# Optimization experiments

Hardware: AMD Instinct MI355X
Metric: run time of the kernel (lower is better)

The kernel has to match this reference:

```python
import jax, jax.numpy as jnp
import numpy as np

B, L1, L2, H = 32, 512, 512, 1024
NEG_INF = jnp.float32(-1e30)


def setup_inputs() -> dict:
    key = jax.random.key(0)
    k1, k2, k3, k4 = jax.random.split(key, 4)
    x1_bar = jax.random.normal(k1, (B, L1, H), dtype=jnp.float32)
    x2_bar = jax.random.normal(k2, (B, L2, H), dtype=jnp.float32)
    # lengths in [1, L] to avoid fully-masked (NaN) rows
    seq_lengths1 = jax.random.randint(k3, (B,), 1, L1 + 1, dtype=jnp.int32)
    seq_lengths2 = jax.random.randint(k4, (B,), 1, L2 + 1, dtype=jnp.int32)
    return {"x1_bar": x1_bar, "seq_lengths1": seq_lengths1,
            "x2_bar": x2_bar, "seq_lengths2": seq_lengths2}


def _enhance(x_bar, x_tilde):
    return jnp.concatenate([x_bar, x_tilde, x_bar - x_tilde, x_bar * x_tilde], axis=-1)


def reference(x1_bar, seq_lengths1, x2_bar, seq_lengths2):
    # e[b, i, j] = x1_bar[b, i] . x2_bar[b, j]
    e = jnp.einsum('bih,bjh->bij', x1_bar, x2_bar)  # [B, L1, L2]
    # mask_k[b, l] True where position l is padding (l >= length)
    mask1 = jnp.arange(x1_bar.shape[1])[None, :] >= seq_lengths1[:, None]  # [B, L1]
    mask2 = jnp.arange(x2_bar.shape[1])[None, :] >= seq_lengths2[:, None]  # [B, L2]
    # attend x1 -> x2: softmax over j with padded j masked
    a12 = jax.nn.softmax(jnp.where(mask2[:, None, :], NEG_INF, e), axis=2)  # [B, L1, L2]
    x1_tilde = jnp.einsum('bij,bjh->bih', a12, x2_bar)
    # attend x2 -> x1: softmax over i (on e^T) with padded i masked
    a21 = jax.nn.softmax(jnp.where(mask1[:, None, :], NEG_INF, e.transpose(0, 2, 1)), axis=2)  # [B, L2, L1]
    x2_tilde = jnp.einsum('bji,bih->bjh', a21, x1_bar)
    return _enhance(x1_bar, x1_tilde), _enhance(x2_bar, x2_tilde)
```

## Files before the change

### kernel.cpp

```cpp
#include <hip/hip_runtime.h>
#include <math.h>


namespace {

constexpr int BATCH = 32;
constexpr int L = 512;
constexpr int H = 1024;
constexpr int OUTH = 4 * H;

constexpr int BM = 128;
constexpr int BN = 128;
constexpr int KT = 32;
constexpr int LDSP = BM + 4;

__device__ __forceinline__ float wave_max(float v) {
#pragma unroll
  for (int off = 32; off > 0; off >>= 1) v = fmaxf(v, __shfl_xor(v, off));
  return v;
}
__device__ __forceinline__ float wave_sum(float v) {
#pragma unroll
  for (int off = 32; off > 0; off >>= 1) v += __shfl_xor(v, off);
  return v;
}

__global__ __launch_bounds__(256, 2)
void gemm_nt_kernel(const float* __restrict__ A, const float* __restrict__ Bm,
                    float* __restrict__ C) {
  __shared__ __align__(16) float As[KT][LDSP];
  __shared__ __align__(16) float Bs[KT][LDSP];
  const int b = blockIdx.z;
  const int m0 = blockIdx.x * BM;
  const int n0 = blockIdx.y * BN;
  const int tid = threadIdx.x;
  const float* Ab = A + (size_t)b * L * H + (size_t)m0 * H;
  const float* Bb = Bm + (size_t)b * L * H + (size_t)n0 * H;

  const int srow = tid >> 1;
  const int soff = (tid & 1) << 4;

  const int tm = tid & 15;
  const int tn = tid >> 4;

  float c[8][8];
#pragma unroll
  for (int i = 0; i < 8; ++i)
#pragma unroll
    for (int j = 0; j < 8; ++j) c[i][j] = 0.f;

  for (int k0 = 0; k0 < H; k0 += KT) {
    float4 av[4], bv[4];
    const float4* ap = (const float4*)(Ab + (size_t)srow * H + k0 + soff);
    const float4* bp = (const float4*)(Bb + (size_t)srow * H + k0 + soff);
#pragma unroll
    for (int q = 0; q < 4; ++q) av[q] = ap[q];
#pragma unroll
    for (int q = 0; q < 4; ++q) bv[q] = bp[q];
    __syncthreads();
#pragma unroll
    for (int q = 0; q < 4; ++q) {
      As[soff + q * 4 + 0][srow] = av[q].x;
      As[soff + q * 4 + 1][srow] = av[q].y;
      As[soff + q * 4 + 2][srow] = av[q].z;
      As[soff + q * 4 + 3][srow] = av[q].w;
      Bs[soff + q * 4 + 0][srow] = bv[q].x;
      Bs[soff + q * 4 + 1][srow] = bv[q].y;
      Bs[soff + q * 4 + 2][srow] = bv[q].z;
      Bs[soff + q * 4 + 3][srow] = bv[q].w;
    }
    __syncthreads();
#pragma unroll
    for (int k = 0; k < KT; ++k) {
      float a[8], bb[8];
      *(float4*)&a[0] = *(const float4*)&As[k][tm * 4];
      *(float4*)&a[4] = *(const float4*)&As[k][64 + tm * 4];
      *(float4*)&bb[0] = *(const float4*)&Bs[k][tn * 4];
      *(float4*)&bb[4] = *(const float4*)&Bs[k][64 + tn * 4];
#pragma unroll
      for (int i = 0; i < 8; ++i)
#pragma unroll
        for (int j = 0; j < 8; ++j) c[i][j] = fmaf(a[i], bb[j], c[i][j]);
    }
  }

  float* Cb = C + (size_t)b * L * L;
#pragma unroll
  for (int i = 0; i < 8; ++i) {
    const int m = m0 + ((i < 4) ? (tm * 4 + i) : (64 + tm * 4 + (i - 4)));
    float4 v0 = make_float4(c[i][0], c[i][1], c[i][2], c[i][3]);
    float4 v1 = make_float4(c[i][4], c[i][5], c[i][6], c[i][7]);
    *(float4*)(Cb + (size_t)m * L + n0 + tn * 4) = v0;
    *(float4*)(Cb + (size_t)m * L + n0 + 64 + tn * 4) = v1;
  }
}

__global__ __launch_bounds__(256)
void col_stats_partial_kernel(const float* __restrict__ e, const int* __restrict__ len1,
                              float* __restrict__ pm, float* __restrict__ ps) {
  const int b = blockIdx.y;
  const int j = blockIdx.x * 256 + threadIdx.x;
  const int ch = blockIdx.z;
  const int n1 = len1[b];
  const int i0 = ch * (L / 4);
  const int i1 = min(n1, i0 + L / 4);
  const float* eb = e + (size_t)b * L * L + j;
  float m = -INFINITY, s = 0.f;
  for (int i = i0; i < i1; ++i) {
    float v = eb[(size_t)i * L];
    float nm = fmaxf(m, v);
    s = s * __expf(m - nm) + __expf(v - nm);
    m = nm;
  }
  const int idx = (ch * BATCH + b) * L + j;
  pm[idx] = m;
  ps[idx] = s;
}

__global__ __launch_bounds__(256)
void col_stats_combine_kernel(const float* __restrict__ pm, const float* __restrict__ ps,
                              float* __restrict__ cmax, float* __restrict__ crcp) {
  const int idx = blockIdx.x * 256 + threadIdx.x;
  float m = -INFINITY;
#pragma unroll
  for (int c = 0; c < 4; ++c) m = fmaxf(m, pm[c * (BATCH * L) + idx]);
  float s = 0.f;
#pragma unroll
  for (int c = 0; c < 4; ++c) {
    float mc = pm[c * (BATCH * L) + idx];
    float sc = ps[c * (BATCH * L) + idx];
    s += (mc == -INFINITY) ? 0.f : sc * __expf(mc - m);
  }
  cmax[idx] = m;
  crcp[idx] = 1.f / s;
}

__global__ __launch_bounds__(256)
void transpose_softmax_kernel(const float* __restrict__ e, const float* __restrict__ cmax,
                              const float* __restrict__ crcp, const int* __restrict__ len1,
                              float* __restrict__ p21) {
  __shared__ float t[64][65];
  const int b = blockIdx.z;
  const int i0 = blockIdx.x << 6;
  const int j0 = blockIdx.y << 6;
  const int cc = threadIdx.x & 63;
  const int rr = threadIdx.x >> 6;
  const float* eb = e + (size_t)b * L * L;
#pragma unroll
  for (int ch = 0; ch < 16; ++ch) {
    const int r = (ch << 2) + rr;
    t[r][cc] = eb[(size_t)(i0 + r) * L + j0 + cc];
  }
  __syncthreads();
  const int n1 = len1[b];
  float* pb = p21 + (size_t)b * L * L;
#pragma unroll
  for (int ch = 0; ch < 16; ++ch) {
    const int r = (ch << 2) + rr;
    const int j = j0 + r;
    const float mj = cmax[b * L + j];
    const float rj = crcp[b * L + j];
    const int i = i0 + cc;
    const float val = (i < n1) ? __expf(t[cc][r] - mj) * rj : 0.f;
    pb[(size_t)j * L + i] = val;
  }
}

__global__ __launch_bounds__(256)
void row_softmax_kernel(float* __restrict__ e, const int* __restrict__ len2) {
  const int wave = (blockIdx.x << 2) + (threadIdx.x >> 6);
  const int lane = threadIdx.x & 63;
  const int b = wave >> 9;
  const int i = wave & (L - 1);
  const int n2 = len2[b];
  float* row = e + ((size_t)b * L + i) * L;
  float v[8];
  float m = -INFINITY;
#pragma unroll
  for (int q = 0; q < 8; ++q) {
    const int j = (q << 6) + lane;
    v[q] = row[j];
    if (j < n2) m = fmaxf(m, v[q]);
  }
  m = wave_max(m);
  float s = 0.f;
#pragma unroll
  for (int q = 0; q < 8; ++q) {
    const int j = (q << 6) + lane;
    v[q] = (j < n2) ? __expf(v[q] - m) : 0.f;
    s += v[q];
  }
  s = wave_sum(s);
  const float r = 1.f / s;
#pragma unroll
  for (int q = 0; q < 8; ++q) row[(q << 6) + lane] = v[q] * r;
}

__global__ __launch_bounds__(256, 2)
void gemm_nn_out_kernel(const float* __restrict__ P, const float* __restrict__ X,
                        const float* __restrict__ Xbar, float* __restrict__ Out) {
  __shared__ __align__(16) float As[KT][LDSP];
  __shared__ __align__(16) float Bs[KT][LDSP];
  const int b = blockIdx.z;
  const int m0 = blockIdx.x * BM;
  const int n0 = blockIdx.y * BN;
  const int tid = threadIdx.x;
  const float* Pb = P + (size_t)b * L * L + (size_t)m0 * L;
  const float* Xb = X + (size_t)b * L * H;

  const int srow = tid >> 1;
  const int soff = (tid & 1) << 4;
  const int bk = tid & 31;
  const int bseg = (tid >> 5) << 4;

  const int tm = tid & 15;
  const int tn = tid >> 4;

  float c[8][8];
#pragma unroll
  for (int i = 0; i < 8; ++i)
#pragma unroll
    for (int j = 0; j < 8; ++j) c[i][j] = 0.f;

  for (int k0 = 0; k0 < L; k0 += KT) {
    float4 av[4], bv[4];
    const float4* ap = (const float4*)(Pb + (size_t)srow * L + k0 + soff);
    const float4* bp = (const float4*)(Xb + (size_t)(k0 + bk) * H + n0 + bseg);
#pragma unroll
    for (int q = 0; q < 4; ++q) av[q] = ap[q];
#pragma unroll
    for (int q = 0; q < 4; ++q) bv[q] = bp[q];
    __syncthreads();
#pragma unroll
    for (int q = 0; q < 4; ++q) {
      As[soff + q * 4 + 0][srow] = av[q].x;
      As[soff + q * 4 + 1][srow] = av[q].y;
      As[soff + q * 4 + 2][srow] = av[q].z;
      As[soff + q * 4 + 3][srow] = av[q].w;
    }
#pragma unroll
    for (int q = 0; q < 4; ++q) *(float4*)&Bs[bk][bseg + q * 4] = bv[q];
    __syncthreads();
#pragma unroll
    for (int k = 0; k < KT; ++k) {
      float a[8], bb[8];
      *(float4*)&a[0] = *(const float4*)&As[k][tm * 4];
      *(float4*)&a[4] = *(const float4*)&As[k][64 + tm * 4];
      *(float4*)&bb[0] = *(const float4*)&Bs[k][tn * 4];
      *(float4*)&bb[4] = *(const float4*)&Bs[k][64 + tn * 4];
#pragma unroll
      for (int i = 0; i < 8; ++i)
#pragma unroll
        for (int j = 0; j < 8; ++j) c[i][j] = fmaf(a[i], bb[j], c[i][j]);
    }
  }

  const float* XbarB = Xbar + (size_t)b * L * H;
  float* OutB = Out + (size_t)b * L * OUTH;
#pragma unroll
  for (int i = 0; i < 8; ++i) {
    const int m = m0 + ((i < 4) ? (tm * 4 + i) : (64 + tm * 4 + (i - 4)));
    const float* xr = XbarB + (size_t)m * H;
    float* orow = OutB + (size_t)m * OUTH;
    const int na = n0 + tn * 4;
    const int nb = n0 + 64 + tn * 4;
    const float4 xb0 = *(const float4*)(xr + na);
    const float4 xb1 = *(const float4*)(xr + nb);
    const float4 t0 = make_float4(c[i][0], c[i][1], c[i][2], c[i][3]);
    const float4 t1 = make_float4(c[i][4], c[i][5], c[i][6], c[i][7]);
    *(float4*)(orow + na) = xb0;
    *(float4*)(orow + nb) = xb1;
    *(float4*)(orow + H + na) = t0;
    *(float4*)(orow + H + nb) = t1;
    *(float4*)(orow + 2 * H + na) = make_float4(xb0.x - t0.x, xb0.y - t0.y, xb0.z - t0.z, xb0.w - t0.w);
    *(float4*)(orow + 2 * H + nb) = make_float4(xb1.x - t1.x, xb1.y - t1.y, xb1.z - t1.z, xb1.w - t1.w);
    *(float4*)(orow + 3 * H + na) = make_float4(xb0.x * t0.x, xb0.y * t0.y, xb0.z * t0.z, xb0.w * t0.w);
    *(float4*)(orow + 3 * H + nb) = make_float4(xb1.x * t1.x, xb1.y * t1.y, xb1.z * t1.z, xb1.w * t1.w);
  }
}

}

extern "C" void kernel_launch(void* const* d_in, const int* in_sizes, int n_in,
                              void* d_out, int out_size, void* d_ws, size_t ws_size,
                              hipStream_t stream) {
  (void)in_sizes; (void)n_in; (void)out_size; (void)ws_size;
  const float* x1 = (const float*)d_in[0];
  const int* len1 = (const int*)d_in[1];
  const float* x2 = (const float*)d_in[2];
  const int* len2 = (const int*)d_in[3];
  float* out = (float*)d_out;

  float* ws = (float*)d_ws;
  const size_t EL = (size_t)BATCH * L * L;
  float* e = ws;
  float* p21 = ws + EL;
  float* pm = ws + 2 * EL;
  float* psv = pm + 4 * BATCH * L;
  float* cm = psv + 4 * BATCH * L;
  float* cr = cm + BATCH * L;

  const dim3 blk(256);

  gemm_nt_kernel<<<dim3(L / BM, L / BN, BATCH), blk, 0, stream>>>(x1, x2, e);
  col_stats_partial_kernel<<<dim3(L / 256, BATCH, 4), blk, 0, stream>>>(e, len1, pm, psv);
  col_stats_combine_kernel<<<dim3(BATCH * L / 256), blk, 0, stream>>>(pm, psv, cm, cr);
  transpose_softmax_kernel<<<dim3(L / 64, L / 64, BATCH), blk, 0, stream>>>(e, cm, cr, len1, p21);
  row_softmax_kernel<<<dim3(BATCH * L / 4), blk, 0, stream>>>(e, len2);
  gemm_nn_out_kernel<<<dim3(L / BM, H / BN, BATCH), blk, 0, stream>>>(e, x2, x1, out);
  gemm_nn_out_kernel<<<dim3(L / BM, H / BN, BATCH), blk, 0, stream>>>(
      p21, x1, x2, out + (size_t)BATCH * L * OUTH);
}
```

Measured before the change: 1.288 ms.

## Use split-bf16 MFMA GEMMs with pre-converted hi/lo operands

Replaces the FP32 FMA GEMMs with bf16 MFMA GEMMs. Each fp32 value is split into a high and a low bf16 part, and three MFMA products (hh, hl, lh) recover near-fp32 accuracy. New conversion kernels write bf16 hi/lo copies of the inputs and transposed copies of them, and the softmax kernels emit bf16 hi/lo probabilities directly. Operands are staged with global_load_lds. This moves the dominant GEMM work onto the matrix cores, at the cost of extra conversion passes, more workspace memory, and a slight loss of accuracy from dropping the lo*lo term.

```diff
diff --git a/kernel.cpp b/kernel.cpp
--- a/kernel.cpp
+++ b/kernel.cpp
@@ -1,4 +1,5 @@
 #include <hip/hip_runtime.h>
+#include <hip/hip_bf16.h>
 #include <math.h>
 
 
@@ -8,11 +9,24 @@
 constexpr int L = 512;
 constexpr int H = 1024;
 constexpr int OUTH = 4 * H;
-
-constexpr int BM = 128;
-constexpr int BN = 128;
-constexpr int KT = 32;
-constexpr int LDSP = BM + 4;
+constexpr size_t NLH = (size_t)BATCH * L * H;
+constexpr size_t NLL = (size_t)BATCH * L * L;
+
+typedef short bf16x8 __attribute__((ext_vector_type(8)));
+typedef float f32x4 __attribute__((ext_vector_type(4)));
+
+__device__ __forceinline__ void split_bf16(float v, short& h, short& l) {
+  __hip_bfloat16 bh = __float2bfloat16(v);
+  float r = v - __bfloat162float(bh);
+  __hip_bfloat16 bl = __float2bfloat16(r);
+  h = __builtin_bit_cast(short, bh);
+  l = __builtin_bit_cast(short, bl);
+}
+
+__device__ __forceinline__ void gload_lds16(const short* g, short* l) {
+  __builtin_amdgcn_global_load_lds((const __attribute__((address_space(1))) void*)g,
+                                   (__attribute__((address_space(3))) void*)l, 16, 0, 0);
+}
 
 __device__ __forceinline__ float wave_max(float v) {
 #pragma unroll
@@ -25,74 +39,134 @@
   return v;
 }
 
-__global__ __launch_bounds__(256, 2)
-void gemm_nt_kernel(const float* __restrict__ A, const float* __restrict__ Bm,
-                    float* __restrict__ C) {
-  __shared__ __align__(16) float As[KT][LDSP];
-  __shared__ __align__(16) float Bs[KT][LDSP];
+__global__ __launch_bounds__(256)
+void convert_kernel(const float* __restrict__ x, short* __restrict__ hi,
+                    short* __restrict__ lo) {
+  const size_t t = (size_t)blockIdx.x * 256 + threadIdx.x;
+  const float4 a = *((const float4*)x + t * 2);
+  const float4 b = *((const float4*)x + t * 2 + 1);
+  const float vs[8] = {a.x, a.y, a.z, a.w, b.x, b.y, b.z, b.w};
+  bf16x8 hv, lv;
+#pragma unroll
+  for (int e = 0; e < 8; ++e) {
+    short hs, ls;
+    split_bf16(vs[e], hs, ls);
+    hv[e] = hs;
+    lv[e] = ls;
+  }
+  *(bf16x8*)(hi + t * 8) = hv;
+  *(bf16x8*)(lo + t * 8) = lv;
+}
+
+__global__ __launch_bounds__(256)
+void convt_kernel(const float* __restrict__ x, short* __restrict__ hiT,
+                  short* __restrict__ loT) {
+  __shared__ float t[64][65];
   const int b = blockIdx.z;
-  const int m0 = blockIdx.x * BM;
-  const int n0 = blockIdx.y * BN;
-  const int tid = threadIdx.x;
-  const float* Ab = A + (size_t)b * L * H + (size_t)m0 * H;
-  const float* Bb = Bm + (size_t)b * L * H + (size_t)n0 * H;
-
-  const int srow = tid >> 1;
-  const int soff = (tid & 1) << 4;
-
-  const int tm = tid & 15;
-  const int tn = tid >> 4;
-
-  float c[8][8];
-#pragma unroll
-  for (int i = 0; i < 8; ++i)
-#pragma unroll
-    for (int j = 0; j < 8; ++j) c[i][j] = 0.f;
-
-  for (int k0 = 0; k0 < H; k0 += KT) {
-    float4 av[4], bv[4];
-    const float4* ap = (const float4*)(Ab + (size_t)srow * H + k0 + soff);
-    const float4* bp = (const float4*)(Bb + (size_t)srow * H + k0 + soff);
-#pragma unroll
-    for (int q = 0; q < 4; ++q) av[q] = ap[q];
-#pragma unroll
-    for (int q = 0; q < 4; ++q) bv[q] = bp[q];
+  const int l0 = blockIdx.x << 6;
+  const int h0 = blockIdx.y << 6;
+  const int c = threadIdx.x & 63;
+  const int rr = threadIdx.x >> 6;
+  const float* xb = x + (size_t)b * L * H;
+#pragma unroll
+  for (int q = 0; q < 16; ++q) {
+    const int r = (q << 2) + rr;
+    t[r][c] = xb[(size_t)(l0 + r) * H + h0 + c];
+  }
+  __syncthreads();
+  const int hr = threadIdx.x >> 2;
+  const int c2 = threadIdx.x & 3;
+  bf16x8 h0v, h1v, l0v, l1v;
+#pragma unroll
+  for (int e = 0; e < 16; ++e) {
+    short hs, ls;
+    split_bf16(t[c2 * 16 + e][hr], hs, ls);
+    if (e < 8) { h0v[e] = hs; l0v[e] = ls; }
+    else       { h1v[e - 8] = hs; l1v[e - 8] = ls; }
+  }
+  const size_t ob = (size_t)b * H * L + (size_t)(h0 + hr) * L + l0 + c2 * 16;
+  *(bf16x8*)(hiT + ob) = h0v;
+  *(bf16x8*)(hiT + ob + 8) = h1v;
+  *(bf16x8*)(loT + ob) = l0v;
+  *(bf16x8*)(loT + ob + 8) = l1v;
+}
+
+template <int KSTEPS>
+__device__ __forceinline__ void gemm_core(const short* __restrict__ Ahi,
+                                          const short* __restrict__ Alo, int lda,
+                                          int arow0, const short* __restrict__ Bhi,
+                                          const short* __restrict__ Blo, int ldb,
+                                          int brow0, short* lds, f32x4 (&acc)[4][4],
+                                          int wr, int wc, int lane, int wave) {
+  const int rsub = lane >> 2;
+  const int ksub = (lane & 3) * 8;
+  const int fr = lane & 15;
+  const int ko = (lane >> 4) * 8;
+  for (int ks = 0; ks < KSTEPS; ++ks) {
+    const int k0 = ks * 32;
     __syncthreads();
 #pragma unroll
-    for (int q = 0; q < 4; ++q) {
-      As[soff + q * 4 + 0][srow] = av[q].x;
-      As[soff + q * 4 + 1][srow] = av[q].y;
-      As[soff + q * 4 + 2][srow] = av[q].z;
-      As[soff + q * 4 + 3][srow] = av[q].w;
-      Bs[soff + q * 4 + 0][srow] = bv[q].x;
-      Bs[soff + q * 4 + 1][srow] = bv[q].y;
-      Bs[soff + q * 4 + 2][srow] = bv[q].z;
-      Bs[soff + q * 4 + 3][srow] = bv[q].w;
+    for (int b2 = 0; b2 < 4; ++b2) {
+#pragma unroll
+      for (int s2 = 0; s2 < 2; ++s2) {
+        const int sub = s2 * 4 + wave;
+        const int row = sub * 16 + rsub;
+        const short* g;
+        if (b2 == 0)      g = Ahi + (size_t)(arow0 + row) * lda + k0 + ksub;
+        else if (b2 == 1) g = Alo + (size_t)(arow0 + row) * lda + k0 + ksub;
+        else if (b2 == 2) g = Bhi + (size_t)(brow0 + row) * ldb + k0 + ksub;
+        else              g = Blo + (size_t)(brow0 + row) * ldb + k0 + ksub;
+        gload_lds16(g, lds + b2 * 4096 + sub * 512);
+      }
     }
     __syncthreads();
-#pragma unroll
-    for (int k = 0; k < KT; ++k) {
-      float a[8], bb[8];
-      *(float4*)&a[0] = *(const float4*)&As[k][tm * 4];
-      *(float4*)&a[4] = *(const float4*)&As[k][64 + tm * 4];
-      *(float4*)&bb[0] = *(const float4*)&Bs[k][tn * 4];
-      *(float4*)&bb[4] = *(const float4*)&Bs[k][64 + tn * 4];
-#pragma unroll
-      for (int i = 0; i < 8; ++i)
-#pragma unroll
-        for (int j = 0; j < 8; ++j) c[i][j] = fmaf(a[i], bb[j], c[i][j]);
+    bf16x8 ah[4], al[4], bh[4], bl[4];
+#pragma unroll
+    for (int q = 0; q < 4; ++q) {
+      const int ar = wr * 64 + q * 16 + fr;
+      const int br = wc * 64 + q * 16 + fr;
+      ah[q] = *(const bf16x8*)(lds + 0 * 4096 + ar * 32 + ko);
+      al[q] = *(const bf16x8*)(lds + 1 * 4096 + ar * 32 + ko);
+      bh[q] = *(const bf16x8*)(lds + 2 * 4096 + br * 32 + ko);
+      bl[q] = *(const bf16x8*)(lds + 3 * 4096 + br * 32 + ko);
     }
-  }
-
-  float* Cb = C + (size_t)b * L * L;
-#pragma unroll
-  for (int i = 0; i < 8; ++i) {
-    const int m = m0 + ((i < 4) ? (tm * 4 + i) : (64 + tm * 4 + (i - 4)));
-    float4 v0 = make_float4(c[i][0], c[i][1], c[i][2], c[i][3]);
-    float4 v1 = make_float4(c[i][4], c[i][5], c[i][6], c[i][7]);
-    *(float4*)(Cb + (size_t)m * L + n0 + tn * 4) = v0;
-    *(float4*)(Cb + (size_t)m * L + n0 + 64 + tn * 4) = v1;
-  }
+#pragma unroll
+    for (int q = 0; q < 4; ++q)
+#pragma unroll
+      for (int r = 0; r < 4; ++r) {
+        acc[q][r] = __builtin_amdgcn_mfma_f32_16x16x32_bf16(ah[q], bh[r], acc[q][r], 0, 0, 0);
+        acc[q][r] = __builtin_amdgcn_mfma_f32_16x16x32_bf16(ah[q], bl[r], acc[q][r], 0, 0, 0);
+        acc[q][r] = __builtin_amdgcn_mfma_f32_16x16x32_bf16(al[q], bh[r], acc[q][r], 0, 0, 0);
+      }
+  }
+}
+
+__global__ __launch_bounds__(256, 2)
+void egemm_kernel(const short* __restrict__ x1h, const short* __restrict__ x1l,
+                  const short* __restrict__ x2h, const short* __restrict__ x2l,
+                  float* __restrict__ e) {
+  __shared__ short lds[4 * 4096];
+  const int b = blockIdx.z;
+  const int m0 = blockIdx.x * 128;
+  const int n0 = blockIdx.y * 128;
+  const int lane = threadIdx.x & 63;
+  const int wave = threadIdx.x >> 6;
+  const int wr = wave >> 1, wc = wave & 1;
+  f32x4 acc[4][4] = {};
+  const size_t ib = (size_t)b * L * H;
+  gemm_core<H / 32>(x1h + ib, x1l + ib, H, m0, x2h + ib, x2l + ib, H, n0, lds, acc,
+                    wr, wc, lane, wave);
+  float* eb = e + (size_t)b * L * L;
+  const int cr = (lane >> 4) * 4;
+  const int cc = lane & 15;
+#pragma unroll
+  for (int q = 0; q < 4; ++q)
+#pragma unroll
+    for (int r = 0; r < 4; ++r)
+#pragma unroll
+      for (int v = 0; v < 4; ++v)
+        eb[(size_t)(m0 + wr * 64 + q * 16 + cr + v) * L + n0 + wc * 64 + r * 16 + cc] =
+            acc[q][r][v];
 }
 
 __global__ __launch_bounds__(256)
@@ -136,147 +210,117 @@
 }
 
 __global__ __launch_bounds__(256)
-void transpose_softmax_kernel(const float* __restrict__ e, const float* __restrict__ cmax,
-                              const float* __restrict__ crcp, const int* __restrict__ len1,
-                              float* __restrict__ p21) {
+void tsoftmax_kernel(const float* __restrict__ e, const float* __restrict__ cmax,
+                     const float* __restrict__ crcp, const int* __restrict__ len1,
+                     short* __restrict__ p21h, short* __restrict__ p21l) {
   __shared__ float t[64][65];
   const int b = blockIdx.z;
   const int i0 = blockIdx.x << 6;
   const int j0 = blockIdx.y << 6;
-  const int cc = threadIdx.x & 63;
+  const int c = threadIdx.x & 63;
   const int rr = threadIdx.x >> 6;
   const float* eb = e + (size_t)b * L * L;
 #pragma unroll
-  for (int ch = 0; ch < 16; ++ch) {
-    const int r = (ch << 2) + rr;
-    t[r][cc] = eb[(size_t)(i0 + r) * L + j0 + cc];
+  for (int q = 0; q < 16; ++q) {
+    const int r = (q << 2) + rr;
+    t[r][c] = eb[(size_t)(i0 + r) * L + j0 + c];
   }
   __syncthreads();
   const int n1 = len1[b];
-  float* pb = p21 + (size_t)b * L * L;
-#pragma unroll
-  for (int ch = 0; ch < 16; ++ch) {
-    const int r = (ch << 2) + rr;
-    const int j = j0 + r;
-    const float mj = cmax[b * L + j];
-    const float rj = crcp[b * L + j];
-    const int i = i0 + cc;
-    const float val = (i < n1) ? __expf(t[cc][r] - mj) * rj : 0.f;
-    pb[(size_t)j * L + i] = val;
-  }
-}
-
-__global__ __launch_bounds__(256)
-void row_softmax_kernel(float* __restrict__ e, const int* __restrict__ len2) {
+  const int jr = threadIdx.x >> 2;
+  const int c2 = threadIdx.x & 3;
+  const int j = j0 + jr;
+  const float mj = cmax[b * L + j];
+  const float rj = crcp[b * L + j];
+  bf16x8 h0v, h1v, l0v, l1v;
+#pragma unroll
+  for (int e2 = 0; e2 < 16; ++e2) {
+    const int i = i0 + c2 * 16 + e2;
+    const float p = (i < n1) ? __expf(t[c2 * 16 + e2][jr] - mj) * rj : 0.f;
+    short hs, ls;
+    split_bf16(p, hs, ls);
+    if (e2 < 8) { h0v[e2] = hs; l0v[e2] = ls; }
+    else        { h1v[e2 - 8] = hs; l1v[e2 - 8] = ls; }
+  }
+  const size_t ob = (size_t)b * L * L + (size_t)j * L + i0 + c2 * 16;
+  *(bf16x8*)(p21h + ob) = h0v;
+  *(bf16x8*)(p21h + ob + 8) = h1v;
+  *(bf16x8*)(p21l + ob) = l0v;
+  *(bf16x8*)(p21l + ob + 8) = l1v;
+}
+
+__global__ __launch_bounds__(256)
+void rsoftmax_kernel(const float* __restrict__ e, const int* __restrict__ len2,
+                     short* __restrict__ p12h, short* __restrict__ p12l) {
   const int wave = (blockIdx.x << 2) + (threadIdx.x >> 6);
   const int lane = threadIdx.x & 63;
   const int b = wave >> 9;
   const int i = wave & (L - 1);
   const int n2 = len2[b];
-  float* row = e + ((size_t)b * L + i) * L;
-  float v[8];
+  const size_t rowb = ((size_t)b * L + i) * L;
+  const float4 a = *(const float4*)(e + rowb + lane * 8);
+  const float4 c = *(const float4*)(e + rowb + lane * 8 + 4);
+  float v[8] = {a.x, a.y, a.z, a.w, c.x, c.y, c.z, c.w};
   float m = -INFINITY;
 #pragma unroll
-  for (int q = 0; q < 8; ++q) {
-    const int j = (q << 6) + lane;
-    v[q] = row[j];
-    if (j < n2) m = fmaxf(m, v[q]);
-  }
+  for (int q = 0; q < 8; ++q)
+    if (lane * 8 + q < n2) m = fmaxf(m, v[q]);
   m = wave_max(m);
   float s = 0.f;
 #pragma unroll
   for (int q = 0; q < 8; ++q) {
-    const int j = (q << 6) + lane;
-    v[q] = (j < n2) ? __expf(v[q] - m) : 0.f;
+    v[q] = (lane * 8 + q < n2) ? __expf(v[q] - m) : 0.f;
     s += v[q];
   }
   s = wave_sum(s);
   const float r = 1.f / s;
-#pragma unroll
-  for (int q = 0; q < 8; ++q) row[(q << 6) + lane] = v[q] * r;
+  bf16x8 hv, lv;
+#pragma unroll
+  for (int q = 0; q < 8; ++q) {
+    short hs, ls;
+    split_bf16(v[q] * r, hs, ls);
+    hv[q] = hs;
+    lv[q] = ls;
+  }
+  *(bf16x8*)(p12h + rowb + lane * 8) = hv;
+  *(bf16x8*)(p12l + rowb + lane * 8) = lv;
 }
 
 __global__ __launch_bounds__(256, 2)
-void gemm_nn_out_kernel(const float* __restrict__ P, const float* __restrict__ X,
-                        const float* __restrict__ Xbar, float* __restrict__ Out) {
-  __shared__ __align__(16) float As[KT][LDSP];
-  __shared__ __align__(16) float Bs[KT][LDSP];
+void ogemm_kernel(const short* __restrict__ ph, const short* __restrict__ pl,
+                  const short* __restrict__ xth, const short* __restrict__ xtl,
+                  const float* __restrict__ xbar, float* __restrict__ outp) {
+  __shared__ short lds[4 * 4096];
   const int b = blockIdx.z;
-  const int m0 = blockIdx.x * BM;
-  const int n0 = blockIdx.y * BN;
-  const int tid = threadIdx.x;
-  const float* Pb = P + (size_t)b * L * L + (size_t)m0 * L;
-  const float* Xb = X + (size_t)b * L * H;
-
-  const int srow = tid >> 1;
-  const int soff = (tid & 1) << 4;
-  const int bk = tid & 31;
-  const int bseg = (tid >> 5) << 4;
-
-  const int tm = tid & 15;
-  const int tn = tid >> 4;
-
-  float c[8][8];
-#pragma unroll
-  for (int i = 0; i < 8; ++i)
-#pragma unroll
-    for (int j = 0; j < 8; ++j) c[i][j] = 0.f;
-
-  for (int k0 = 0; k0 < L; k0 += KT) {
-    float4 av[4], bv[4];
-    const float4* ap = (const float4*)(Pb + (size_t)srow * L + k0 + soff);
-    const float4* bp = (const float4*)(Xb + (size_t)(k0 + bk) * H + n0 + bseg);
-#pragma unroll
-    for (int q = 0; q < 4; ++q) av[q] = ap[q];
-#pragma unroll
-    for (int q = 0; q < 4; ++q) bv[q] = bp[q];
-    __syncthreads();
-#pragma unroll
-    for (int q = 0; q < 4; ++q) {
-      As[soff + q * 4 + 0][srow] = av[q].x;
-      As[soff + q * 4 + 1][srow] = av[q].y;
-      As[soff + q * 4 + 2][srow] = av[q].z;
-      As[soff + q * 4 + 3][srow] = av[q].w;
-    }
-#pragma unroll
-    for (int q = 0; q < 4; ++q) *(float4*)&Bs[bk][bseg + q * 4] = bv[q];
-    __syncthreads();
-#pragma unroll
-    for (int k = 0; k < KT; ++k) {
-      float a[8], bb[8];
-      *(float4*)&a[0] = *(const float4*)&As[k][tm * 4];
-      *(float4*)&a[4] = *(const float4*)&As[k][64 + tm * 4];
-      *(float4*)&bb[0] = *(const float4*)&Bs[k][tn * 4];
-      *(float4*)&bb[4] = *(const float4*)&Bs[k][64 + tn * 4];
-#pragma unroll
-      for (int i = 0; i < 8; ++i)
-#pragma unroll
-        for (int j = 0; j < 8; ++j) c[i][j] = fmaf(a[i], bb[j], c[i][j]);
-    }
-  }
-
-  const float* XbarB = Xbar + (size_t)b * L * H;
-  float* OutB = Out + (size_t)b * L * OUTH;
-#pragma unroll
-  for (int i = 0; i < 8; ++i) {
-    const int m = m0 + ((i < 4) ? (tm * 4 + i) : (64 + tm * 4 + (i - 4)));
-    const float* xr = XbarB + (size_t)m * H;
-    float* orow = OutB + (size_t)m * OUTH;
-    const int na = n0 + tn * 4;
-    const int nb = n0 + 64 + tn * 4;
-    const float4 xb0 = *(const float4*)(xr + na);
-    const float4 xb1 = *(const float4*)(xr + nb);
-    const float4 t0 = make_float4(c[i][0], c[i][1], c[i][2], c[i][3]);
-    const float4 t1 = make_float4(c[i][4], c[i][5], c[i][6], c[i][7]);
-    *(float4*)(orow + na) = xb0;
-    *(float4*)(orow + nb) = xb1;
-    *(float4*)(orow + H + na) = t0;
-    *(float4*)(orow + H + nb) = t1;
-    *(float4*)(orow + 2 * H + na) = make_float4(xb0.x - t0.x, xb0.y - t0.y, xb0.z - t0.z, xb0.w - t0.w);
-    *(float4*)(orow + 2 * H + nb) = make_float4(xb1.x - t1.x, xb1.y - t1.y, xb1.z - t1.z, xb1.w - t1.w);
-    *(float4*)(orow + 3 * H + na) = make_float4(xb0.x * t0.x, xb0.y * t0.y, xb0.z * t0.z, xb0.w * t0.w);
-    *(float4*)(orow + 3 * H + nb) = make_float4(xb1.x * t1.x, xb1.y * t1.y, xb1.z * t1.z, xb1.w * t1.w);
-  }
+  const int m0 = blockIdx.x * 128;
+  const int n0 = blockIdx.y * 128;
+  const int lane = threadIdx.x & 63;
+  const int wave = threadIdx.x >> 6;
+  const int wr = wave >> 1, wc = wave & 1;
+  f32x4 acc[4][4] = {};
+  gemm_core<L / 32>(ph + (size_t)b * L * L, pl + (size_t)b * L * L, L, m0,
+                    xth + (size_t)b * H * L, xtl + (size_t)b * H * L, L, n0, lds, acc,
+                    wr, wc, lane, wave);
+  const float* xbb = xbar + (size_t)b * L * H;
+  float* ob = outp + (size_t)b * L * OUTH;
+  const int cr = (lane >> 4) * 4;
+  const int cc = lane & 15;
+#pragma unroll
+  for (int q = 0; q < 4; ++q)
+#pragma unroll
+    for (int r = 0; r < 4; ++r)
+#pragma unroll
+      for (int v = 0; v < 4; ++v) {
+        const int i = m0 + wr * 64 + q * 16 + cr + v;
+        const int h = n0 + wc * 64 + r * 16 + cc;
+        const float xb = xbb[(size_t)i * H + h];
+        const float tv = acc[q][r][v];
+        float* orow = ob + (size_t)i * OUTH;
+        orow[h] = xb;
+        orow[H + h] = tv;
+        orow[2 * H + h] = xb - tv;
+        orow[3 * H + h] = xb * tv;
+      }
 }
 
 }
@@ -291,23 +335,41 @@
   const int* len2 = (const int*)d_in[3];
   float* out = (float*)d_out;
 
-  float* ws = (float*)d_ws;
-  const size_t EL = (size_t)BATCH * L * L;
-  float* e = ws;
-  float* p21 = ws + EL;
-  float* pm = ws + 2 * EL;
+  short* wsS = (short*)d_ws;
+  short* x1h = wsS;
+  short* x1l = x1h + NLH;
+  short* x2h = x1l + NLH;
+  short* x2l = x2h + NLH;
+  short* x1Th = x2l + NLH;
+  short* x1Tl = x1Th + NLH;
+  short* x2Th = x1Tl + NLH;
+  short* x2Tl = x2Th + NLH;
+  float* e = (float*)(x2Tl + NLH);
+  short* p12h = (short*)(e + NLL);
+  short* p12l = p12h + NLL;
+  short* p21h = p12l + NLL;
+  short* p21l = p21h + NLL;
+  float* pm = (float*)(p21l + NLL);
   float* psv = pm + 4 * BATCH * L;
   float* cm = psv + 4 * BATCH * L;
   float* cr = cm + BATCH * L;
 
   const dim3 blk(256);
-
-  gemm_nt_kernel<<<dim3(L / BM, L / BN, BATCH), blk, 0, stream>>>(x1, x2, e);
+  const int cvtBlocks = (int)(NLH / 8 / 256);
+
+  convert_kernel<<<cvtBlocks, blk, 0, stream>>>(x1, x1h, x1l);
+  convert_kernel<<<cvtBlocks, blk, 0, stream>>>(x2, x2h, x2l);
+  convt_kernel<<<dim3(L / 64, H / 64, BATCH), blk, 0, stream>>>(x1, x1Th, x1Tl);
+  convt_kernel<<<dim3(L / 64, H / 64, BATCH), blk, 0, stream>>>(x2, x2Th, x2Tl);
+
+  egemm_kernel<<<dim3(L / 128, L / 128, BATCH), blk, 0, stream>>>(x1h, x1l, x2h, x2l, e);
+
   col_stats_partial_kernel<<<dim3(L / 256, BATCH, 4), blk, 0, stream>>>(e, len1, pm, psv);
   col_stats_combine_kernel<<<dim3(BATCH * L / 256), blk, 0, stream>>>(pm, psv, cm, cr);
-  transpose_softmax_kernel<<<dim3(L / 64, L / 64, BATCH), blk, 0, stream>>>(e, cm, cr, len1, p21);
-  row_softmax_kernel<<<dim3(BATCH * L / 4), blk, 0, stream>>>(e, len2);
-  gemm_nn_out_kernel<<<dim3(L / BM, H / BN, BATCH), blk, 0, stream>>>(e, x2, x1, out);
-  gemm_nn_out_kernel<<<dim3(L / BM, H / BN, BATCH), blk, 0, stream>>>(
-      p21, x1, x2, out + (size_t)BATCH * L * OUTH);
-}
+  tsoftmax_kernel<<<dim3(L / 64, L / 64, BATCH), blk, 0, stream>>>(e, cm, cr, len1, p21h, p21l);
+  rsoftmax_kernel<<<dim3(BATCH * L / 4), blk, 0, stream>>>(e, len2, p12h, p12l);
+
+  ogemm_kernel<<<dim3(L / 128, H / 128, BATCH), blk, 0, stream>>>(p12h, p12l, x2Th, x2Tl, x1, out);
+  ogemm_kernel<<<dim3(L / 128, H / 128, BATCH), blk, 0, stream>>>(p21h, p21l, x1Th, x1Tl, x2,
+                                                                  out + NLH * 4);
+}
```

After: 1.071 ms. 16.8% less time.
